# Kernel tuning notes

Hardware: AMD Instinct MI355X
Metric: run time of the kernel (lower is better)

Reference implementation:

```python
import jax, jax.numpy as jnp
import numpy as np

N_QUBITS = 4
N_LAYERS = 3
LETTERS = "ijkl"  # one axis label per qubit; batch axis is 'b'
CNOT = np.array([[1, 0, 0, 0], [0, 1, 0, 0], [0, 0, 0, 1], [0, 0, 1, 0]], dtype=np.complex64).reshape(2, 2, 2, 2)


def _apply_1q(state, U, w, batched):
    # state: [B,2,2,2,2]; U: [2,2] (shared) or [B,2,2] (per-sample)
    s = "b" + LETTERS
    t = LETTERS[w]
    u = ("b" if batched else "") + "z" + t
    return jnp.einsum(f"{u},{s}->{s.replace(t, 'z')}", U, state)


def _apply_cnot(state, c, t):
    s = "b" + LETTERS
    a, b = LETTERS[c], LETTERS[t]
    out = s.replace(a, "x").replace(b, "y")
    return jnp.einsum(f"xy{a}{b},{s}->{out}", jnp.asarray(CNOT), state)


def _rx(theta):
    # theta: [B] -> batched RX gates [B,2,2]
    c = jnp.cos(theta / 2).astype(jnp.complex64)
    s = (-1j * jnp.sin(theta / 2)).astype(jnp.complex64)
    return jnp.stack([jnp.stack([c, s], -1), jnp.stack([s, c], -1)], -2)


def _rz(a):
    e = jnp.exp(-1j * a.astype(jnp.complex64) / 2)
    zero = jnp.zeros((), jnp.complex64)
    return jnp.array([[e, zero], [zero, jnp.conj(e)]])


def _ry(a):
    c = jnp.cos(a / 2).astype(jnp.complex64)
    s = jnp.sin(a / 2).astype(jnp.complex64)
    return jnp.array([[c, -s], [s, c]])


def _rot(phi, theta, omega):
    # PennyLane Rot = RZ(omega) @ RY(theta) @ RZ(phi)
    return _rz(omega) @ _ry(theta) @ _rz(phi)


def _circuit(qparams, z):
    # qparams: [n_layers, n_qubits, 3] float32; z: [B, n_qubits] float32
    B = z.shape[0]
    state = jnp.zeros((B,) + (2,) * N_QUBITS, jnp.complex64)
    state = state.at[:, 0, 0, 0, 0].set(1.0 + 0.0j)
    # data-encoding RX layer (per-sample angles -> batched gates)
    for w in range(N_QUBITS):
        state = _apply_1q(state, _rx(z[:, w]), w, batched=True)
    # variational layers: Rot on every wire then CNOT ladder
    for layer in range(N_LAYERS):
        for w in range(N_QUBITS):
            U = _rot(qparams[layer, w, 0], qparams[layer, w, 1], qparams[layer, w, 2])
            state = _apply_1q(state, U, w, batched=False)
        for w in range(N_QUBITS - 1):
            state = _apply_cnot(state, w, w + 1)
    probs = jnp.abs(state) ** 2  # [B,2,2,2,2] float32
    zsign = jnp.array([1.0, -1.0], jnp.float32)
    s = "b" + LETTERS
    evs = [jnp.einsum(f"{s},{LETTERS[w]}->b", probs, zsign) for w in range(N_QUBITS)]
    return jnp.stack(evs, axis=-1)  # [B, n_qubits]


def reference(x, enc_w, enc_b, qparams, cls_w, cls_b, bn_gamma, bn_beta):
    B = x.shape[0]
    # avg_pool2d(kernel_size=6) on 28x28 -> 4x4 (floor division drops last 4 rows/cols)
    pooled = x[:, :, :24, :24].reshape(B, 1, 4, 6, 4, 6).mean(axis=(3, 5)).reshape(B, 16)
    z = pooled @ enc_w.T + enc_b  # [B, n_qubits]
    evs = _circuit(qparams, z)    # [B, n_qubits]
    out = evs @ cls_w.T + cls_b   # [B, output_dim]
    # BatchNorm1d in training mode: biased batch statistics, eps=1e-5
    mu = out.mean(axis=0)
    var = ((out - mu) ** 2).mean(axis=0)
    out = (out - mu) / jnp.sqrt(var + 1e-5) * bn_gamma + bn_beta
    return out


def setup_inputs() -> dict:
    key = jax.random.key(0)
    ks = jax.random.split(key, 6)
    B = 32768
    return {
        "x": jax.random.normal(ks[0], (B, 1, 28, 28), jnp.float32),
        "enc_w": jax.random.normal(ks[1], (N_QUBITS, 16), jnp.float32) * 0.25,
        "enc_b": jnp.zeros((N_QUBITS,), jnp.float32),
        "qparams": jax.random.normal(ks[2], (N_LAYERS, N_QUBITS, 3), jnp.float32),
        "cls_w": jax.random.normal(ks[3], (4, N_QUBITS), jnp.float32) * 0.5,
        "cls_b": jnp.zeros((4,), jnp.float32),
        "bn_gamma": jnp.ones((4,), jnp.float32),
        "bn_beta": jnp.zeros((4,), jnp.float32),
    }
```

## Files before the change

kernel.cpp:

```cpp
#include <hip/hip_runtime.h>
#include <math.h>


#define BTOT 32768

__global__ __launch_bounds__(64) void prep_kernel(
    const float* __restrict__ qparams, const float* __restrict__ cls_w,
    float* __restrict__ Vr, float* __restrict__ Vi, float* __restrict__ W2)
{
    int t = threadIdx.x;
    if (t < 16) {
        float pr[16], pi[16];
        #pragma unroll
        for (int i = 0; i < 16; ++i) { pr[i] = (i == t) ? 1.f : 0.f; pi[i] = 0.f; }
        for (int layer = 0; layer < 3; ++layer) {
            for (int w = 0; w < 4; ++w) {
                const float* qp = qparams + (layer * 4 + w) * 3;
                float phi = qp[0], th = qp[1], om = qp[2];
                float c, s, ca, sa, cd, sd;
                sincosf(0.5f * th, &s, &c);
                sincosf(0.5f * (phi + om), &sa, &ca);
                sincosf(0.5f * (phi - om), &sd, &cd);
                float u00r =  c * ca, u00i = -c * sa;
                float u01r = -s * cd, u01i = -s * sd;
                float u10r =  s * cd, u10i = -s * sd;
                float u11r =  c * ca, u11i =  c * sa;
                int m = 8 >> w;
                for (int idx = 0; idx < 16; ++idx) {
                    if (idx & m) continue;
                    int i1 = idx | m;
                    float ar = pr[idx], ai = pi[idx], br = pr[i1], bi = pi[i1];
                    pr[idx] = u00r*ar - u00i*ai + u01r*br - u01i*bi;
                    pi[idx] = u00r*ai + u00i*ar + u01r*bi + u01i*br;
                    pr[i1]  = u10r*ar - u10i*ai + u11r*br - u11i*bi;
                    pi[i1]  = u10r*ai + u10i*ar + u11r*bi + u11i*br;
                }
            }
            for (int w = 0; w < 3; ++w) {
                int mc = 8 >> w, mt = 8 >> (w + 1);
                for (int idx = 0; idx < 16; ++idx) {
                    if ((idx & mc) && !(idx & mt)) {
                        int i1 = idx | mt;
                        float tr = pr[idx], ti = pi[idx];
                        pr[idx] = pr[i1]; pi[idx] = pi[i1];
                        pr[i1] = tr;      pi[i1] = ti;
                    }
                }
            }
        }
        int p = __popc(t) & 3;
        #pragma unroll
        for (int i = 0; i < 16; ++i) {
            float re = pr[i], im = pi[i], vr, vi;
            if (p == 0)      { vr = re;  vi = im;  }
            else if (p == 1) { vr = im;  vi = -re; }
            else if (p == 2) { vr = -re; vi = -im; }
            else             { vr = -im; vi = re;  }
            Vr[i * 16 + t] = vr;
            Vi[i * 16 + t] = vi;
        }
    }
    {
        int j = t >> 4, i = t & 15;
        float acc = 0.f;
        #pragma unroll
        for (int w = 0; w < 4; ++w) {
            float sgn = (i & (8 >> w)) ? -1.f : 1.f;
            acc += cls_w[j * 4 + w] * sgn;
        }
        W2[j * 16 + i] = acc;
    }
}

__global__ __launch_bounds__(256) void pool_kernel(
    const float* __restrict__ x, float* __restrict__ pooled)
{
    int t = blockIdx.x * 256 + threadIdx.x;
    int s = t >> 4, cell = t & 15;
    const float* base = x + (size_t)s * 784 + (size_t)((cell >> 2) * 6) * 28 + (cell & 3) * 6;
    float sum = 0.f;
    #pragma unroll
    for (int r = 0; r < 6; ++r) {
        const float* rp = base + r * 28;
        sum += (rp[0] + rp[1]) + (rp[2] + rp[3]) + (rp[4] + rp[5]);
    }
    pooled[t] = sum * (1.f / 36.f);
}

__global__ __launch_bounds__(128) void circuit_kernel(
    const float* __restrict__ pooled,
    const float* __restrict__ enc_w, const float* __restrict__ enc_b,
    const float* __restrict__ Vr, const float* __restrict__ Vi,
    const float* __restrict__ W2, const float* __restrict__ cls_b,
    float* __restrict__ preBN, float* __restrict__ sums)
{
    int s = blockIdx.x * 128 + threadIdx.x;
    float pv[16];
    const float4* pp = (const float4*)(pooled + (size_t)s * 16);
    #pragma unroll
    for (int q = 0; q < 4; ++q) {
        float4 v = pp[q];
        pv[q*4+0] = v.x; pv[q*4+1] = v.y; pv[q*4+2] = v.z; pv[q*4+3] = v.w;
    }
    float cz[4], szn[4];
    #pragma unroll
    for (int j = 0; j < 4; ++j) {
        float z = enc_b[j];
        #pragma unroll
        for (int k = 0; k < 16; ++k) z += enc_w[j * 16 + k] * pv[k];
        sincosf(0.5f * z, &szn[j], &cz[j]);
    }
    float a01[4] = {cz[0]*cz[1], cz[0]*szn[1], szn[0]*cz[1], szn[0]*szn[1]};
    float a23[4] = {cz[2]*cz[3], cz[2]*szn[3], szn[2]*cz[3], szn[2]*szn[3]};
    float r[16];
    #pragma unroll
    for (int k = 0; k < 16; ++k) r[k] = a01[k >> 2] * a23[k & 3];
    float out[4] = {cls_b[0], cls_b[1], cls_b[2], cls_b[3]};
    #pragma unroll
    for (int i = 0; i < 16; ++i) {
        float ar = 0.f, ai = 0.f;
        #pragma unroll
        for (int k = 0; k < 16; ++k) {
            ar += Vr[i * 16 + k] * r[k];
            ai += Vi[i * 16 + k] * r[k];
        }
        float p = ar * ar + ai * ai;
        #pragma unroll
        for (int j = 0; j < 4; ++j) out[j] += W2[j * 16 + i] * p;
    }
    ((float4*)preBN)[s] = make_float4(out[0], out[1], out[2], out[3]);

    float v[8] = {out[0], out[1], out[2], out[3],
                  out[0]*out[0], out[1]*out[1], out[2]*out[2], out[3]*out[3]};
    #pragma unroll
    for (int off = 32; off > 0; off >>= 1) {
        #pragma unroll
        for (int m = 0; m < 8; ++m) v[m] += __shfl_down(v[m], off, 64);
    }
    __shared__ float red[2][8];
    int wave = threadIdx.x >> 6, lane = threadIdx.x & 63;
    if (lane == 0) {
        #pragma unroll
        for (int m = 0; m < 8; ++m) red[wave][m] = v[m];
    }
    __syncthreads();
    if (threadIdx.x < 8) atomicAdd(&sums[threadIdx.x], red[0][threadIdx.x] + red[1][threadIdx.x]);
}

__global__ __launch_bounds__(128) void bn_kernel(
    const float* __restrict__ sums,
    const float* __restrict__ gamma, const float* __restrict__ beta,
    float* __restrict__ out)
{
    int s = blockIdx.x * 128 + threadIdx.x;
    const float invB = 1.f / (float)BTOT;
    float4 v = ((const float4*)out)[s];
    float o[4] = {v.x, v.y, v.z, v.w};
    #pragma unroll
    for (int j = 0; j < 4; ++j) {
        float mu   = sums[j] * invB;
        float var  = sums[4 + j] * invB - mu * mu;
        float rstd = rsqrtf(var + 1e-5f);
        o[j] = (o[j] - mu) * rstd * gamma[j] + beta[j];
    }
    ((float4*)out)[s] = make_float4(o[0], o[1], o[2], o[3]);
}

extern "C" void kernel_launch(void* const* d_in, const int* in_sizes, int n_in,
                              void* d_out, int out_size, void* d_ws, size_t ws_size,
                              hipStream_t stream)
{
    const float* x        = (const float*)d_in[0];
    const float* enc_w    = (const float*)d_in[1];
    const float* enc_b    = (const float*)d_in[2];
    const float* qparams  = (const float*)d_in[3];
    const float* cls_w    = (const float*)d_in[4];
    const float* cls_b    = (const float*)d_in[5];
    const float* bn_gamma = (const float*)d_in[6];
    const float* bn_beta  = (const float*)d_in[7];

    float* ws     = (float*)d_ws;
    float* Vr     = ws;
    float* Vi     = ws + 256;
    float* W2     = ws + 512;
    float* sums   = ws + 576;
    float* pooled = ws + 1024;
    float* outp   = (float*)d_out;

    prep_kernel<<<1, 64, 0, stream>>>(qparams, cls_w, Vr, Vi, W2);
    pool_kernel<<<2048, 256, 0, stream>>>(x, pooled);
    hipMemsetAsync(sums, 0, 8 * sizeof(float), stream);
    circuit_kernel<<<256, 128, 0, stream>>>(pooled, enc_w, enc_b, Vr, Vi, W2, cls_b, outp, sums);
    bn_kernel<<<256, 128, 0, stream>>>(sums, bn_gamma, bn_beta, outp);
}
```

Before: 196.7 us.

## Fuse prep, pooling and circuit into one kernel with per-row-group threads

Merges the unitary-precompute, avg-pool and circuit kernels into a single kernel. Each block recomputes the 16x16 unitary into shared memory, and four threads per sample each pool one 6-row band with float4 loads. The threads then combine encoder dot products and the output projection through lane shuffles. This removes the pooled intermediate round-trip and two launches, and spreads the circuit matvec across four threads. In exchange every block redundantly runs the serial 16-thread unitary build, which other threads wait for at a barrier.

```diff
diff --git a/kernel.cpp b/kernel.cpp
--- a/kernel.cpp
+++ b/kernel.cpp
@@ -4,15 +4,32 @@
 
 #define BTOT 32768
 
-__global__ __launch_bounds__(64) void prep_kernel(
-    const float* __restrict__ qparams, const float* __restrict__ cls_w,
-    float* __restrict__ Vr, float* __restrict__ Vi, float* __restrict__ W2)
+__global__ __launch_bounds__(256) void fused_kernel(
+    const float* __restrict__ x,
+    const float* __restrict__ enc_w, const float* __restrict__ enc_b,
+    const float* __restrict__ qparams,
+    const float* __restrict__ cls_w, const float* __restrict__ cls_b,
+    float* __restrict__ preBN, float* __restrict__ sums)
 {
-    int t = threadIdx.x;
-    if (t < 16) {
+    __shared__ float sVrT[256];
+    __shared__ float sViT[256];
+    __shared__ float sW2[64];
+    __shared__ float red[4][8];
+
+    const int tid = threadIdx.x;
+
+    if (tid < 64) {
+        int j = tid >> 4, i = tid & 15;
+        float acc = 0.f;
+        #pragma unroll
+        for (int w = 0; w < 4; ++w)
+            acc += cls_w[j * 4 + w] * ((i & (8 >> w)) ? -1.f : 1.f);
+        sW2[j * 16 + i] = acc;
+    }
+    if (tid < 16) {
         float pr[16], pi[16];
         #pragma unroll
-        for (int i = 0; i < 16; ++i) { pr[i] = (i == t) ? 1.f : 0.f; pi[i] = 0.f; }
+        for (int i = 0; i < 16; ++i) { pr[i] = (i == tid) ? 1.f : 0.f; pi[i] = 0.f; }
         for (int layer = 0; layer < 3; ++layer) {
             for (int w = 0; w < 4; ++w) {
                 const float* qp = qparams + (layer * 4 + w) * 3;
@@ -48,7 +65,7 @@
                 }
             }
         }
-        int p = __popc(t) & 3;
+        int p = __popc(tid) & 3;
         #pragma unroll
         for (int i = 0; i < 16; ++i) {
             float re = pr[i], im = pi[i], vr, vi;
@@ -56,103 +73,101 @@
             else if (p == 1) { vr = im;  vi = -re; }
             else if (p == 2) { vr = -re; vi = -im; }
             else             { vr = -im; vi = re;  }
-            Vr[i * 16 + t] = vr;
-            Vi[i * 16 + t] = vi;
+            sVrT[tid * 16 + i] = vr;
+            sViT[tid * 16 + i] = vi;
         }
     }
-    {
-        int j = t >> 4, i = t & 15;
+
+    const int tg = blockIdx.x * 256 + tid;
+    const int s  = tg >> 2, rg = tg & 3;
+    const float* base = x + (size_t)s * 784 + rg * 6 * 28;
+    float p0 = 0.f, p1 = 0.f, p2 = 0.f, p3 = 0.f;
+    #pragma unroll
+    for (int r = 0; r < 6; ++r) {
+        const float4* rp = (const float4*)(base + r * 28);
+        float4 v0 = rp[0], v1 = rp[1], v2 = rp[2], v3 = rp[3], v4 = rp[4], v5 = rp[5];
+        p0 += (v0.x + v0.y) + (v0.z + v0.w) + (v1.x + v1.y);
+        p1 += (v1.z + v1.w) + (v2.x + v2.y) + (v2.z + v2.w);
+        p2 += (v3.x + v3.y) + (v3.z + v3.w) + (v4.x + v4.y);
+        p3 += (v4.z + v4.w) + (v5.x + v5.y) + (v5.z + v5.w);
+    }
+    const float inv36 = 1.f / 36.f;
+    float pv[4] = {p0 * inv36, p1 * inv36, p2 * inv36, p3 * inv36};
+
+    float z[4];
+    #pragma unroll
+    for (int j = 0; j < 4; ++j) {
         float acc = 0.f;
         #pragma unroll
-        for (int w = 0; w < 4; ++w) {
-            float sgn = (i & (8 >> w)) ? -1.f : 1.f;
-            acc += cls_w[j * 4 + w] * sgn;
-        }
-        W2[j * 16 + i] = acc;
-    }
+        for (int c = 0; c < 4; ++c) acc += enc_w[j * 16 + rg * 4 + c] * pv[c];
+        z[j] = acc;
+    }
+    #pragma unroll
+    for (int j = 0; j < 4; ++j) {
+        z[j] += __shfl_xor(z[j], 1, 64);
+        z[j] += __shfl_xor(z[j], 2, 64);
+        z[j] += enc_b[j];
+    }
+
+    float cz[4], sz[4];
+    #pragma unroll
+    for (int j = 0; j < 4; ++j) sincosf(0.5f * z[j], &sz[j], &cz[j]);
+    float a01[4] = {cz[0]*cz[1], cz[0]*sz[1], sz[0]*cz[1], sz[0]*sz[1]};
+    float a23[4] = {cz[2]*cz[3], cz[2]*sz[3], sz[2]*cz[3], sz[2]*sz[3]};
+    float rv[16];
+    #pragma unroll
+    for (int k = 0; k < 16; ++k) rv[k] = a01[k >> 2] * a23[k & 3];
+
+    __syncthreads();
+
+    float arA[4] = {0,0,0,0}, aiA[4] = {0,0,0,0};
+    #pragma unroll
+    for (int k = 0; k < 16; ++k) {
+        float4 vr4 = *(const float4*)&sVrT[k * 16 + rg * 4];
+        float4 vi4 = *(const float4*)&sViT[k * 16 + rg * 4];
+        float rk = rv[k];
+        arA[0] += vr4.x * rk; arA[1] += vr4.y * rk; arA[2] += vr4.z * rk; arA[3] += vr4.w * rk;
+        aiA[0] += vi4.x * rk; aiA[1] += vi4.y * rk; aiA[2] += vi4.z * rk; aiA[3] += vi4.w * rk;
+    }
+    float out[4] = {0, 0, 0, 0};
+    #pragma unroll
+    for (int m = 0; m < 4; ++m) {
+        float pp = arA[m] * arA[m] + aiA[m] * aiA[m];
+        #pragma unroll
+        for (int j = 0; j < 4; ++j) out[j] += sW2[j * 16 + rg * 4 + m] * pp;
+    }
+    #pragma unroll
+    for (int j = 0; j < 4; ++j) {
+        out[j] += __shfl_xor(out[j], 1, 64);
+        out[j] += __shfl_xor(out[j], 2, 64);
+        out[j] += cls_b[j];
+    }
+    if (rg == 0) ((float4*)preBN)[s] = make_float4(out[0], out[1], out[2], out[3]);
+
+    float w = (rg == 0) ? 1.f : 0.f;
+    float v8[8] = {out[0]*w, out[1]*w, out[2]*w, out[3]*w,
+                   out[0]*out[0]*w, out[1]*out[1]*w, out[2]*out[2]*w, out[3]*out[3]*w};
+    #pragma unroll
+    for (int off = 32; off > 0; off >>= 1) {
+        #pragma unroll
+        for (int m = 0; m < 8; ++m) v8[m] += __shfl_down(v8[m], off, 64);
+    }
+    int wave = tid >> 6, lane = tid & 63;
+    if (lane == 0) {
+        #pragma unroll
+        for (int m = 0; m < 8; ++m) red[wave][m] = v8[m];
+    }
+    __syncthreads();
+    if (tid < 8)
+        atomicAdd(&sums[tid], red[0][tid] + red[1][tid] + red[2][tid] + red[3][tid]);
 }
 
-__global__ __launch_bounds__(256) void pool_kernel(
-    const float* __restrict__ x, float* __restrict__ pooled)
-{
-    int t = blockIdx.x * 256 + threadIdx.x;
-    int s = t >> 4, cell = t & 15;
-    const float* base = x + (size_t)s * 784 + (size_t)((cell >> 2) * 6) * 28 + (cell & 3) * 6;
-    float sum = 0.f;
-    #pragma unroll
-    for (int r = 0; r < 6; ++r) {
-        const float* rp = base + r * 28;
-        sum += (rp[0] + rp[1]) + (rp[2] + rp[3]) + (rp[4] + rp[5]);
-    }
-    pooled[t] = sum * (1.f / 36.f);
-}
-
-__global__ __launch_bounds__(128) void circuit_kernel(
-    const float* __restrict__ pooled,
-    const float* __restrict__ enc_w, const float* __restrict__ enc_b,
-    const float* __restrict__ Vr, const float* __restrict__ Vi,
-    const float* __restrict__ W2, const float* __restrict__ cls_b,
-    float* __restrict__ preBN, float* __restrict__ sums)
-{
-    int s = blockIdx.x * 128 + threadIdx.x;
-    float pv[16];
-    const float4* pp = (const float4*)(pooled + (size_t)s * 16);
-    #pragma unroll
-    for (int q = 0; q < 4; ++q) {
-        float4 v = pp[q];
-        pv[q*4+0] = v.x; pv[q*4+1] = v.y; pv[q*4+2] = v.z; pv[q*4+3] = v.w;
-    }
-    float cz[4], szn[4];
-    #pragma unroll
-    for (int j = 0; j < 4; ++j) {
-        float z = enc_b[j];
-        #pragma unroll
-        for (int k = 0; k < 16; ++k) z += enc_w[j * 16 + k] * pv[k];
-        sincosf(0.5f * z, &szn[j], &cz[j]);
-    }
-    float a01[4] = {cz[0]*cz[1], cz[0]*szn[1], szn[0]*cz[1], szn[0]*szn[1]};
-    float a23[4] = {cz[2]*cz[3], cz[2]*szn[3], szn[2]*cz[3], szn[2]*szn[3]};
-    float r[16];
-    #pragma unroll
-    for (int k = 0; k < 16; ++k) r[k] = a01[k >> 2] * a23[k & 3];
-    float out[4] = {cls_b[0], cls_b[1], cls_b[2], cls_b[3]};
-    #pragma unroll
-    for (int i = 0; i < 16; ++i) {
-        float ar = 0.f, ai = 0.f;
-        #pragma unroll
-        for (int k = 0; k < 16; ++k) {
-            ar += Vr[i * 16 + k] * r[k];
-            ai += Vi[i * 16 + k] * r[k];
-        }
-        float p = ar * ar + ai * ai;
-        #pragma unroll
-        for (int j = 0; j < 4; ++j) out[j] += W2[j * 16 + i] * p;
-    }
-    ((float4*)preBN)[s] = make_float4(out[0], out[1], out[2], out[3]);
-
-    float v[8] = {out[0], out[1], out[2], out[3],
-                  out[0]*out[0], out[1]*out[1], out[2]*out[2], out[3]*out[3]};
-    #pragma unroll
-    for (int off = 32; off > 0; off >>= 1) {
-        #pragma unroll
-        for (int m = 0; m < 8; ++m) v[m] += __shfl_down(v[m], off, 64);
-    }
-    __shared__ float red[2][8];
-    int wave = threadIdx.x >> 6, lane = threadIdx.x & 63;
-    if (lane == 0) {
-        #pragma unroll
-        for (int m = 0; m < 8; ++m) red[wave][m] = v[m];
-    }
-    __syncthreads();
-    if (threadIdx.x < 8) atomicAdd(&sums[threadIdx.x], red[0][threadIdx.x] + red[1][threadIdx.x]);
-}
-
-__global__ __launch_bounds__(128) void bn_kernel(
+__global__ __launch_bounds__(256) void bn_kernel(
     const float* __restrict__ sums,
     const float* __restrict__ gamma, const float* __restrict__ beta,
     float* __restrict__ out)
 {
-    int s = blockIdx.x * 128 + threadIdx.x;
+    int s = blockIdx.x * 256 + threadIdx.x;
     const float invB = 1.f / (float)BTOT;
     float4 v = ((const float4*)out)[s];
     float o[4] = {v.x, v.y, v.z, v.w};
@@ -179,17 +194,11 @@
     const float* bn_gamma = (const float*)d_in[6];
     const float* bn_beta  = (const float*)d_in[7];
 
-    float* ws     = (float*)d_ws;
-    float* Vr     = ws;
-    float* Vi     = ws + 256;
-    float* W2     = ws + 512;
-    float* sums   = ws + 576;
-    float* pooled = ws + 1024;
-    float* outp   = (float*)d_out;
-
-    prep_kernel<<<1, 64, 0, stream>>>(qparams, cls_w, Vr, Vi, W2);
-    pool_kernel<<<2048, 256, 0, stream>>>(x, pooled);
+    float* sums = (float*)d_ws;
+    float* outp = (float*)d_out;
+
     hipMemsetAsync(sums, 0, 8 * sizeof(float), stream);
-    circuit_kernel<<<256, 128, 0, stream>>>(pooled, enc_w, enc_b, Vr, Vi, W2, cls_b, outp, sums);
-    bn_kernel<<<256, 128, 0, stream>>>(sums, bn_gamma, bn_beta, outp);
+    fused_kernel<<<512, 256, 0, stream>>>(x, enc_w, enc_b, qparams, cls_w, cls_b,
+                                          outp, sums);
+    bn_kernel<<<128, 256, 0, stream>>>(sums, bn_gamma, bn_beta, outp);
 }
```

Measured after the change: 185.6 us. 1.06x faster.
